# Kernel optimization log

Hardware: AMD Instinct MI355X
Metric: run time of the kernel (lower is better)

The kernel has to match this reference:

```python
import jax, jax.numpy as jnp
import numpy as np

B, S, H, I, E, TOP_K = 2, 1024, 1024, 2048, 8, 2


def setup_inputs() -> dict:
    key = jax.random.key(0)
    ks = jax.random.split(key, 5)
    return {
        "hidden_states": jax.random.normal(ks[0], (B, S, H), jnp.float32),
        # torch Linear weights are (out, in)
        "router_w": jax.random.normal(ks[1], (E, H), jnp.float32) * 0.02,
        "w1": jax.random.normal(ks[2], (E, I, H), jnp.float32) * 0.02,
        "v": jax.random.normal(ks[3], (E, I, H), jnp.float32) * 0.02,
        "w2": jax.random.normal(ks[4], (E, H, I), jnp.float32) * 0.02,
    }


def _moe(x, router_w, w1, v, w2):
    # x: [T, H] flattened tokens
    T = x.shape[0]
    n_exp = router_w.shape[0]
    logits = x @ router_w.T                                    # [T, E]
    probs = jax.nn.softmax(logits.astype(jnp.float32), axis=-1)
    top_p, top_i = jax.lax.top_k(probs, TOP_K)                 # [T, K]
    top_p = top_p / top_p.sum(axis=-1, keepdims=True)
    top_p = top_p.astype(x.dtype)
    # dense gate matrix [T, E]; zero for unselected experts -> identical math
    # to the torch gather / index_add combine
    gates = jnp.zeros((T, n_exp), x.dtype).at[
        jnp.arange(T)[:, None], top_i].set(top_p)
    out = jnp.zeros_like(x)
    for e in range(n_exp):  # small fixed expert loop keeps peak memory low
        h = jax.nn.gelu(x @ w1[e].T, approximate=False) * (x @ v[e].T)  # [T, I]
        out = out + gates[:, e:e + 1] * (h @ w2[e].T)                   # [T, H]
    return out, logits


def reference(hidden_states, router_w, w1, v, w2):
    b, s, h = hidden_states.shape
    out, logits = _moe(hidden_states.reshape(-1, h), router_w, w1, v, w2)
    return out.reshape(b, s, h), logits
```

## Files before the change

kernel.cpp:

```cpp
#include <hip/hip_runtime.h>
#include <math.h>

#define T 2048
#define HD 1024
#define ID 2048
#define NE 8

typedef short bf16x8 __attribute__((ext_vector_type(8)));
typedef float f32x4 __attribute__((ext_vector_type(4)));
typedef unsigned short u16x8 __attribute__((ext_vector_type(8)));

__device__ __forceinline__ unsigned short f2bf(float f) {
  union { float f; unsigned u; } v; v.f = f;
  unsigned r = v.u + 0x7FFFu + ((v.u >> 16) & 1u);
  return (unsigned short)(r >> 16);
}

__device__ __forceinline__ u16x8 cvt8(float4 a, float4 b) {
  u16x8 o;
  o[0] = f2bf(a.x); o[1] = f2bf(a.y); o[2] = f2bf(a.z); o[3] = f2bf(a.w);
  o[4] = f2bf(b.x); o[5] = f2bf(b.y); o[6] = f2bf(b.z); o[7] = f2bf(b.w);
  return o;
}

__device__ __forceinline__ void cast_chunk16(const float* __restrict__ s,
                                             unsigned short* __restrict__ d,
                                             size_t base) {
  size_t idx = base + (size_t)threadIdx.x * 16;
  float4 f0 = *(const float4*)(s + idx);
  float4 f1 = *(const float4*)(s + idx + 4);
  float4 f2 = *(const float4*)(s + idx + 8);
  float4 f3 = *(const float4*)(s + idx + 12);
  *(u16x8*)(d + idx) = cvt8(f0, f1);
  *(u16x8*)(d + idx + 8) = cvt8(f2, f3);
}

__device__ __forceinline__ void glds16(const unsigned short* g, unsigned short* l) {
  __builtin_amdgcn_global_load_lds(
      (const __attribute__((address_space(1))) unsigned int*)(g),
      (__attribute__((address_space(3))) unsigned int*)(l), 16, 0, 0);
}

__global__ __launch_bounds__(256) void prep_kernel(
    const float* __restrict__ x, const float* __restrict__ rw,
    const float* __restrict__ w1, const float* __restrict__ v,
    unsigned short* __restrict__ xb, unsigned short* __restrict__ w1b,
    unsigned short* __restrict__ vb, float* __restrict__ logits_out,
    int* __restrict__ pair_rowid, float* __restrict__ pair_gate,
    int* __restrict__ counts) {
  int bx = blockIdx.x;
  if (bx >= 1024) {
    int cid = bx - 1024;
    const float* s = (cid < 4096) ? w1 : v;
    unsigned short* d = (cid < 4096) ? w1b : vb;
    cast_chunk16(s, d, (size_t)(cid & 4095) * 4096);
    return;
  }
  if (bx >= 512) {
    cast_chunk16(x, xb, (size_t)(bx - 512) * 4096);
    return;
  }
  __shared__ float rws[NE * HD];
  int tid = threadIdx.x;
  for (int j = tid * 4; j < NE * HD; j += 256 * 4)
    *(float4*)&rws[j] = *(const float4*)&rw[j];
  __syncthreads();
  int wid = tid >> 6, lane = tid & 63;
  int t = bx * 4 + wid;
  float acc[NE];
#pragma unroll
  for (int e = 0; e < NE; e++) acc[e] = 0.f;
  const float* xrow = x + (size_t)t * HD;
  for (int j = 0; j < HD; j += 64) {
    float xv = xrow[j + lane];
#pragma unroll
    for (int e = 0; e < NE; e++) acc[e] += xv * rws[e * HD + j + lane];
  }
#pragma unroll
  for (int e = 0; e < NE; e++)
    for (int off = 32; off > 0; off >>= 1) acc[e] += __shfl_xor(acc[e], off, 64);
  if (lane == 0) {
#pragma unroll
    for (int e = 0; e < NE; e++) logits_out[t * NE + e] = acc[e];
    int e0 = 0;
#pragma unroll
    for (int e = 1; e < NE; e++) if (acc[e] > acc[e0]) e0 = e;
    int e1 = (e0 == 0) ? 1 : 0;
#pragma unroll
    for (int e = 0; e < NE; e++)
      if (e != e0 && e != e1 && acc[e] > acc[e1]) e1 = e;
    float b = __expf(acc[e1] - acc[e0]);
    float g0 = 1.f / (1.f + b);
    float g1 = 1.f - g0;
    int p0 = atomicAdd(&counts[e0], 1);
    pair_rowid[e0 * T + p0] = t * 2;
    pair_gate[e0 * T + p0] = g0;
    int p1 = atomicAdd(&counts[e1], 1);
    pair_rowid[e1 * T + p1] = t * 2 + 1;
    pair_gate[e1 * T + p1] = g1;
  }
}

__global__ __launch_bounds__(256) void gemm1_kernel(
    const unsigned short* __restrict__ xb, const unsigned short* __restrict__ w1b,
    const unsigned short* __restrict__ vb, unsigned short* __restrict__ hb,
    const float* __restrict__ w2, unsigned short* __restrict__ w2b,
    const int* __restrict__ pair_rowid, const int* __restrict__ counts) {
  if (blockIdx.x >= 32) {
    int cid = (blockIdx.x - 32) + 32 * (blockIdx.y + 16 * blockIdx.z);
    cast_chunk16(w2, w2b, (size_t)cid * 4096);
    return;
  }
  int e = blockIdx.z;
  int cnt = counts[e];
  int row0 = blockIdx.y * 128;
  if (row0 >= cnt) return;
  __shared__ unsigned short As[128 * 64];
  __shared__ unsigned short B1s[64 * 64];
  __shared__ unsigned short B2s[64 * 64];
  __shared__ int rids[128];
  int tid = threadIdx.x;
  if (tid < 128) {
    int idx = row0 + tid; if (idx > cnt - 1) idx = cnt - 1;
    rids[tid] = pair_rowid[e * T + idx];
  }
  __syncthreads();
  int lane = tid & 63, wid = tid >> 6;
  int wr = wid >> 1, wc = wid & 1;
  int col0 = blockIdx.x * 64;
  int gr = lane >> 3, gc = lane & 7;
  const unsigned short *aA[4], *aB1[2], *aB2[2];
#pragma unroll
  for (int c = 0; c < 4; c++) {
    int row = (c * 4 + wid) * 8 + gr;
    int tok = rids[row] >> 1;
    aA[c] = xb + (size_t)tok * HD + ((gc ^ (row & 7)) * 8);
  }
#pragma unroll
  for (int c = 0; c < 2; c++) {
    int row = (c * 4 + wid) * 8 + gr;
    int kswz = ((gc ^ (row & 7)) * 8);
    aB1[c] = w1b + ((size_t)(e * ID + col0 + row)) * HD + kswz;
    aB2[c] = vb  + ((size_t)(e * ID + col0 + row)) * HD + kswz;
  }
  f32x4 acc1[4][2] = {};
  f32x4 acc3[4][2] = {};
  int mrow = lane & 15, kq = lane >> 4;
  int swzm = mrow & 7;
  for (int kt = 0; kt < HD; kt += 64) {
#pragma unroll
    for (int c = 0; c < 4; c++)
      glds16(aA[c] + kt, &As[(c * 4 + wid) * 512]);
#pragma unroll
    for (int c = 0; c < 2; c++) {
      glds16(aB1[c] + kt, &B1s[(c * 4 + wid) * 512]);
      glds16(aB2[c] + kt, &B2s[(c * 4 + wid) * 512]);
    }
    __syncthreads();
#pragma unroll
    for (int kk = 0; kk < 2; kk++) {
      int g = kk * 4 + kq;
      int ko = ((g ^ swzm) * 8);
      bf16x8 a[4], b1[2], b2[2];
#pragma unroll
      for (int mi = 0; mi < 4; mi++)
        a[mi] = *(const bf16x8*)&As[(wr * 64 + mi * 16 + mrow) * 64 + ko];
#pragma unroll
      for (int ni = 0; ni < 2; ni++) {
        b1[ni] = *(const bf16x8*)&B1s[(wc * 32 + ni * 16 + mrow) * 64 + ko];
        b2[ni] = *(const bf16x8*)&B2s[(wc * 32 + ni * 16 + mrow) * 64 + ko];
      }
#pragma unroll
      for (int mi = 0; mi < 4; mi++)
#pragma unroll
        for (int ni = 0; ni < 2; ni++) {
          acc1[mi][ni] = __builtin_amdgcn_mfma_f32_16x16x32_bf16(a[mi], b1[ni], acc1[mi][ni], 0, 0, 0);
          acc3[mi][ni] = __builtin_amdgcn_mfma_f32_16x16x32_bf16(a[mi], b2[ni], acc3[mi][ni], 0, 0, 0);
        }
    }
    __syncthreads();
  }
  int dcol = lane & 15, drow4 = (lane >> 4) * 4;
#pragma unroll
  for (int mi = 0; mi < 4; mi++)
#pragma unroll
    for (int ni = 0; ni < 2; ni++)
#pragma unroll
      for (int r = 0; r < 4; r++) {
        int lr = wr * 64 + mi * 16 + drow4 + r;
        if (row0 + lr < cnt) {
          float g1v = acc1[mi][ni][r];
          float g3v = acc3[mi][ni][r];
          float hval = 0.5f * g1v * (1.f + erff(g1v * 0.70710678118654752f)) * g3v;
          int rowid = rids[lr];
          hb[(size_t)rowid * ID + col0 + wc * 32 + ni * 16 + dcol] = f2bf(hval);
        }
      }
}

__global__ __launch_bounds__(256) void gemm2_kernel(
    const unsigned short* __restrict__ hb, const unsigned short* __restrict__ w2b,
    float* __restrict__ out, const int* __restrict__ pair_rowid,
    const float* __restrict__ pair_gate, const int* __restrict__ counts) {
  int e = blockIdx.z;
  int cnt = counts[e];
  int row0 = blockIdx.y * 64;
  if (row0 >= cnt) return;
  __shared__ unsigned short As[64 * 64];
  __shared__ unsigned short Bs[64 * 64];
  __shared__ int rids[64];
  __shared__ float gts[64];
  int tid = threadIdx.x;
  if (tid < 64) {
    int idx = row0 + tid; if (idx > cnt - 1) idx = cnt - 1;
    rids[tid] = pair_rowid[e * T + idx];
    gts[tid] = pair_gate[e * T + idx];
  }
  __syncthreads();
  int lane = tid & 63, wid = tid >> 6;
  int wr = wid >> 1, wc = wid & 1;
  int col0 = blockIdx.x * 64;
  int gr = lane >> 3, gc = lane & 7;
  const unsigned short *aA[2], *aB[2];
#pragma unroll
  for (int c = 0; c < 2; c++) {
    int row = (c * 4 + wid) * 8 + gr;
    int kswz = ((gc ^ (row & 7)) * 8);
    aA[c] = hb  + (size_t)rids[row] * ID + kswz;
    aB[c] = w2b + ((size_t)(e * HD + col0 + row)) * ID + kswz;
  }
  f32x4 acc[2][2] = {};
  int mrow = lane & 15, kq = lane >> 4;
  int swzm = mrow & 7;
  for (int kt = 0; kt < ID; kt += 64) {
#pragma unroll
    for (int c = 0; c < 2; c++) {
      glds16(aA[c] + kt, &As[(c * 4 + wid) * 512]);
      glds16(aB[c] + kt, &Bs[(c * 4 + wid) * 512]);
    }
    __syncthreads();
#pragma unroll
    for (int kk = 0; kk < 2; kk++) {
      int g = kk * 4 + kq;
      int ko = ((g ^ swzm) * 8);
      bf16x8 a[2], b[2];
#pragma unroll
      for (int mi = 0; mi < 2; mi++)
        a[mi] = *(const bf16x8*)&As[(wr * 32 + mi * 16 + mrow) * 64 + ko];
#pragma unroll
      for (int ni = 0; ni < 2; ni++)
        b[ni] = *(const bf16x8*)&Bs[(wc * 32 + ni * 16 + mrow) * 64 + ko];
#pragma unroll
      for (int mi = 0; mi < 2; mi++)
#pragma unroll
        for (int ni = 0; ni < 2; ni++)
          acc[mi][ni] = __builtin_amdgcn_mfma_f32_16x16x32_bf16(a[mi], b[ni], acc[mi][ni], 0, 0, 0);
    }
    __syncthreads();
  }
  int dcol = lane & 15, drow4 = (lane >> 4) * 4;
#pragma unroll
  for (int mi = 0; mi < 2; mi++)
#pragma unroll
    for (int ni = 0; ni < 2; ni++)
#pragma unroll
      for (int r = 0; r < 4; r++) {
        int lr = wr * 32 + mi * 16 + drow4 + r;
        if (row0 + lr < cnt) {
          int tokrow = rids[lr] >> 1;
          float val = gts[lr] * acc[mi][ni][r];
          atomicAdd(&out[(size_t)tokrow * HD + col0 + wc * 32 + ni * 16 + dcol], val);
        }
      }
}

extern "C" void kernel_launch(void* const* d_in, const int* in_sizes, int n_in,
                              void* d_out, int out_size, void* d_ws, size_t ws_size,
                              hipStream_t stream) {
  const float* x  = (const float*)d_in[0];
  const float* rw = (const float*)d_in[1];
  const float* w1 = (const float*)d_in[2];
  const float* v  = (const float*)d_in[3];
  const float* w2 = (const float*)d_in[4];
  float* out = (float*)d_out;
  float* logits_out = out + (size_t)T * HD;

  char* ws = (char*)d_ws;
  unsigned short* xb  = (unsigned short*)(ws);
  unsigned short* hb  = (unsigned short*)(ws + (4u << 20));
  unsigned short* w1b = (unsigned short*)(ws + (20u << 20));
  unsigned short* vb  = (unsigned short*)(ws + (52u << 20));
  unsigned short* w2b = (unsigned short*)(ws + (84u << 20));
  int*   pair_rowid   = (int*)  (ws + (116u << 20));
  float* pair_gate    = (float*)(ws + (116u << 20) + 65536);
  int*   counts       = (int*)  (ws + (116u << 20) + 131072);

  hipMemsetAsync(out, 0, (size_t)T * HD * sizeof(float), stream);
  hipMemsetAsync(counts, 0, NE * sizeof(int), stream);

  prep_kernel<<<9216, 256, 0, stream>>>(x, rw, w1, v, xb, w1b, vb,
                                        logits_out, pair_rowid, pair_gate,
                                        counts);
  gemm1_kernel<<<dim3(ID / 64 + 32, T / 128, NE), 256, 0, stream>>>(
      xb, w1b, vb, hb, w2, w2b, pair_rowid, counts);
  gemm2_kernel<<<dim3(HD / 64, T / 64, NE), 256, 0, stream>>>(
      hb, w2b, out, pair_rowid, pair_gate, counts);
}
```

Before: 368.9 us.

## Replace atomic output scatter with per-pair buffer and combine pass; batch routing atomics

gemm2 now writes each gated (token, expert) row to its own slot in a pair buffer instead of atomically adding into the output. A new combine kernel sums each token's two slots, which removes the output memset and the float atomics. The router now handles 8 tokens per block, reads router weights straight from global memory instead of staging them in LDS, and aggregates per-expert slot reservations into one atomic per expert per block. Expert counters are padded onto separate strides, and the cast loop is rewritten for coalesced float4 access. The pair buffer reuses the w1b workspace region, which is valid only because w1b is dead after gemm1. The change adds an extra kernel launch and an extra pass over the pair buffer.

```diff
diff --git a/kernel.cpp b/kernel.cpp
--- a/kernel.cpp
+++ b/kernel.cpp
@@ -5,10 +5,11 @@
 #define HD 1024
 #define ID 2048
 #define NE 8
+#define CSTRIDE 32
 
 typedef short bf16x8 __attribute__((ext_vector_type(8)));
 typedef float f32x4 __attribute__((ext_vector_type(4)));
-typedef unsigned short u16x8 __attribute__((ext_vector_type(8)));
+typedef unsigned short u16x4 __attribute__((ext_vector_type(4)));
 
 __device__ __forceinline__ unsigned short f2bf(float f) {
   union { float f; unsigned u; } v; v.f = f;
@@ -16,23 +17,17 @@
   return (unsigned short)(r >> 16);
 }
 
-__device__ __forceinline__ u16x8 cvt8(float4 a, float4 b) {
-  u16x8 o;
-  o[0] = f2bf(a.x); o[1] = f2bf(a.y); o[2] = f2bf(a.z); o[3] = f2bf(a.w);
-  o[4] = f2bf(b.x); o[5] = f2bf(b.y); o[6] = f2bf(b.z); o[7] = f2bf(b.w);
-  return o;
-}
-
 __device__ __forceinline__ void cast_chunk16(const float* __restrict__ s,
                                              unsigned short* __restrict__ d,
                                              size_t base) {
-  size_t idx = base + (size_t)threadIdx.x * 16;
-  float4 f0 = *(const float4*)(s + idx);
-  float4 f1 = *(const float4*)(s + idx + 4);
-  float4 f2 = *(const float4*)(s + idx + 8);
-  float4 f3 = *(const float4*)(s + idx + 12);
-  *(u16x8*)(d + idx) = cvt8(f0, f1);
-  *(u16x8*)(d + idx + 8) = cvt8(f2, f3);
+  size_t o = base + (size_t)threadIdx.x * 4;
+#pragma unroll
+  for (int k = 0; k < 4; k++) {
+    float4 f = *(const float4*)(s + o + k * 1024);
+    u16x4 h;
+    h[0] = f2bf(f.x); h[1] = f2bf(f.y); h[2] = f2bf(f.z); h[3] = f2bf(f.w);
+    *(u16x4*)(d + o + k * 1024) = h;
+  }
 }
 
 __device__ __forceinline__ void glds16(const unsigned short* g, unsigned short* l) {
@@ -49,55 +44,70 @@
     int* __restrict__ pair_rowid, float* __restrict__ pair_gate,
     int* __restrict__ counts) {
   int bx = blockIdx.x;
-  if (bx >= 1024) {
-    int cid = bx - 1024;
+  if (bx >= 768) {
+    int cid = bx - 768;
     const float* s = (cid < 4096) ? w1 : v;
     unsigned short* d = (cid < 4096) ? w1b : vb;
     cast_chunk16(s, d, (size_t)(cid & 4095) * 4096);
     return;
   }
-  if (bx >= 512) {
-    cast_chunk16(x, xb, (size_t)(bx - 512) * 4096);
+  if (bx >= 256) {
+    cast_chunk16(x, xb, (size_t)(bx - 256) * 4096);
     return;
   }
-  __shared__ float rws[NE * HD];
+  __shared__ int s_e[16];
+  __shared__ int s_rid[16];
+  __shared__ float s_gt[16];
   int tid = threadIdx.x;
-  for (int j = tid * 4; j < NE * HD; j += 256 * 4)
-    *(float4*)&rws[j] = *(const float4*)&rw[j];
+  int wid = tid >> 6, lane = tid & 63;
+  for (int tk = 0; tk < 2; ++tk) {
+    int t = bx * 8 + wid * 2 + tk;
+    float acc[NE];
+#pragma unroll
+    for (int e = 0; e < NE; e++) acc[e] = 0.f;
+    const float* xrow = x + (size_t)t * HD;
+#pragma unroll 2
+    for (int j = 0; j < HD; j += 64) {
+      float xv = xrow[j + lane];
+#pragma unroll
+      for (int e = 0; e < NE; e++) acc[e] += xv * rw[e * HD + j + lane];
+    }
+#pragma unroll
+    for (int e = 0; e < NE; e++)
+      for (int off = 32; off > 0; off >>= 1) acc[e] += __shfl_xor(acc[e], off, 64);
+    if (lane == 0) {
+#pragma unroll
+      for (int e = 0; e < NE; e++) logits_out[t * NE + e] = acc[e];
+      int e0 = 0;
+#pragma unroll
+      for (int e = 1; e < NE; e++) if (acc[e] > acc[e0]) e0 = e;
+      int e1 = (e0 == 0) ? 1 : 0;
+#pragma unroll
+      for (int e = 0; e < NE; e++)
+        if (e != e0 && e != e1 && acc[e] > acc[e1]) e1 = e;
+      float b = __expf(acc[e1] - acc[e0]);
+      float g0 = 1.f / (1.f + b);
+      float g1 = 1.f - g0;
+      int slot = (wid * 2 + tk) * 2;
+      s_e[slot] = e0; s_rid[slot] = t * 2;     s_gt[slot] = g0;
+      s_e[slot + 1] = e1; s_rid[slot + 1] = t * 2 + 1; s_gt[slot + 1] = g1;
+    }
+  }
   __syncthreads();
-  int wid = tid >> 6, lane = tid & 63;
-  int t = bx * 4 + wid;
-  float acc[NE];
-#pragma unroll
-  for (int e = 0; e < NE; e++) acc[e] = 0.f;
-  const float* xrow = x + (size_t)t * HD;
-  for (int j = 0; j < HD; j += 64) {
-    float xv = xrow[j + lane];
-#pragma unroll
-    for (int e = 0; e < NE; e++) acc[e] += xv * rws[e * HD + j + lane];
-  }
-#pragma unroll
-  for (int e = 0; e < NE; e++)
-    for (int off = 32; off > 0; off >>= 1) acc[e] += __shfl_xor(acc[e], off, 64);
-  if (lane == 0) {
-#pragma unroll
-    for (int e = 0; e < NE; e++) logits_out[t * NE + e] = acc[e];
-    int e0 = 0;
-#pragma unroll
-    for (int e = 1; e < NE; e++) if (acc[e] > acc[e0]) e0 = e;
-    int e1 = (e0 == 0) ? 1 : 0;
-#pragma unroll
-    for (int e = 0; e < NE; e++)
-      if (e != e0 && e != e1 && acc[e] > acc[e1]) e1 = e;
-    float b = __expf(acc[e1] - acc[e0]);
-    float g0 = 1.f / (1.f + b);
-    float g1 = 1.f - g0;
-    int p0 = atomicAdd(&counts[e0], 1);
-    pair_rowid[e0 * T + p0] = t * 2;
-    pair_gate[e0 * T + p0] = g0;
-    int p1 = atomicAdd(&counts[e1], 1);
-    pair_rowid[e1 * T + p1] = t * 2 + 1;
-    pair_gate[e1 * T + p1] = g1;
+  if (tid < NE) {
+    int cnt = 0;
+#pragma unroll
+    for (int k = 0; k < 16; k++) if (s_e[k] == tid) cnt++;
+    if (cnt) {
+      int base = atomicAdd(&counts[tid * CSTRIDE], cnt);
+      int p = 0;
+      for (int k = 0; k < 16; k++)
+        if (s_e[k] == tid) {
+          pair_rowid[tid * T + base + p] = s_rid[k];
+          pair_gate[tid * T + base + p] = s_gt[k];
+          p++;
+        }
+    }
   }
 }
 
@@ -112,7 +122,7 @@
     return;
   }
   int e = blockIdx.z;
-  int cnt = counts[e];
+  int cnt = counts[e * CSTRIDE];
   int row0 = blockIdx.y * 128;
   if (row0 >= cnt) return;
   __shared__ unsigned short As[128 * 64];
@@ -200,10 +210,10 @@
 
 __global__ __launch_bounds__(256) void gemm2_kernel(
     const unsigned short* __restrict__ hb, const unsigned short* __restrict__ w2b,
-    float* __restrict__ out, const int* __restrict__ pair_rowid,
+    float* __restrict__ yb, const int* __restrict__ pair_rowid,
     const float* __restrict__ pair_gate, const int* __restrict__ counts) {
   int e = blockIdx.z;
-  int cnt = counts[e];
+  int cnt = counts[e * CSTRIDE];
   int row0 = blockIdx.y * 64;
   if (row0 >= cnt) return;
   __shared__ unsigned short As[64 * 64];
@@ -267,11 +277,21 @@
       for (int r = 0; r < 4; r++) {
         int lr = wr * 32 + mi * 16 + drow4 + r;
         if (row0 + lr < cnt) {
-          int tokrow = rids[lr] >> 1;
           float val = gts[lr] * acc[mi][ni][r];
-          atomicAdd(&out[(size_t)tokrow * HD + col0 + wc * 32 + ni * 16 + dcol], val);
+          yb[(size_t)rids[lr] * HD + col0 + wc * 32 + ni * 16 + dcol] = val;
         }
       }
+}
+
+__global__ __launch_bounds__(256) void combine_kernel(
+    const float* __restrict__ yb, float* __restrict__ out) {
+  size_t t = blockIdx.x;
+  int c = threadIdx.x * 4;
+  float4 a = *(const float4*)(yb + (t * 2) * HD + c);
+  float4 b = *(const float4*)(yb + (t * 2 + 1) * HD + c);
+  float4 o;
+  o.x = a.x + b.x; o.y = a.y + b.y; o.z = a.z + b.z; o.w = a.w + b.w;
+  *(float4*)(out + t * HD + c) = o;
 }
 
 extern "C" void kernel_launch(void* const* d_in, const int* in_sizes, int n_in,
@@ -291,18 +311,19 @@
   unsigned short* w1b = (unsigned short*)(ws + (20u << 20));
   unsigned short* vb  = (unsigned short*)(ws + (52u << 20));
   unsigned short* w2b = (unsigned short*)(ws + (84u << 20));
+  float* yb           = (float*)(ws + (20u << 20));
   int*   pair_rowid   = (int*)  (ws + (116u << 20));
   float* pair_gate    = (float*)(ws + (116u << 20) + 65536);
   int*   counts       = (int*)  (ws + (116u << 20) + 131072);
 
-  hipMemsetAsync(out, 0, (size_t)T * HD * sizeof(float), stream);
-  hipMemsetAsync(counts, 0, NE * sizeof(int), stream);
-
-  prep_kernel<<<9216, 256, 0, stream>>>(x, rw, w1, v, xb, w1b, vb,
+  hipMemsetAsync(counts, 0, NE * CSTRIDE * sizeof(int), stream);
+
+  prep_kernel<<<8960, 256, 0, stream>>>(x, rw, w1, v, xb, w1b, vb,
                                         logits_out, pair_rowid, pair_gate,
                                         counts);
   gemm1_kernel<<<dim3(ID / 64 + 32, T / 128, NE), 256, 0, stream>>>(
       xb, w1b, vb, hb, w2, w2b, pair_rowid, counts);
   gemm2_kernel<<<dim3(HD / 64, T / 64, NE), 256, 0, stream>>>(
-      hb, w2b, out, pair_rowid, pair_gate, counts);
-}
+      hb, w2b, yb, pair_rowid, pair_gate, counts);
+  combine_kernel<<<T, 256, 0, stream>>>(yb, out);
+}
```

New measurement: 327.7 us. -11.2%, faster.
